# Kernel tuning notes

Hardware: AMD Instinct MI355X
Metric: run time of the kernel (lower is better)

The kernel has to match this reference:

```python
import jax, jax.numpy as jnp
import numpy as np

D = 1024      # embed_dim
E = 2048      # expand * embed_dim
S_DIM = 128   # shrunken attn dim s
C = 256       # chunk size
SRC = 4096    # src_len
G = SRC // C  # num chunks
B = 8
STD = 0.02


def setup_inputs() -> dict:
    key = jax.random.key(0)
    ks = jax.random.split(key, 16)
    n = lambda k, shp: jax.random.normal(k, shp, dtype=jnp.float32)
    inp = {
        "query": n(ks[0], (SRC, B, D)),
        "key":   n(ks[1], (SRC, B, D)),
        "value": n(ks[2], (SRC, B, D)),
        # learned params (torch Linear stored as [in, out])
        "Wxs": n(ks[3], (D, S_DIM)) * STD, "bxs": n(ks[4], (S_DIM,)) * STD,
        "Wve": n(ks[5], (D, E)) * STD,     "bve": n(ks[6], (E,)) * STD,
        "Wue": n(ks[7], (D, E)) * STD,     "bue": n(ks[8], (E,)) * STD,
        "Wod": n(ks[9], (E, D)) * STD,     "bod": n(ks[10], (D,)) * STD,
        "rel_bias": n(ks[11], (C,)) * STD,
        "gamma": n(ks[12], (4, S_DIM)) * STD,
        "beta":  n(ks[13], (4, S_DIM)) * STD,
    }
    return inp


def reference(query, key, value, Wxs, bxs, Wve, bve, Wue, bue, Wod, bod,
              rel_bias, gamma, beta):
    # [S, B, D] -> [B, G, C, D]
    x = jnp.transpose(value, (1, 0, 2)).reshape(B, G, C, D)
    v = jnp.tanh(x @ Wve + bve)          # [b,g,c,e]
    z = jnp.tanh(x @ Wxs + bxs)          # [b,g,c,s]
    q_quad = z * gamma[0] + beta[0]
    k_quad = z * gamma[1] + beta[1]
    q_lin  = z * gamma[2] + beta[2]
    k_lin  = z * gamma[3] + beta[3]
    # local quadratic attention: relu(qk + bias)^2
    qk = jnp.einsum('bgns,bgms->bgnm', q_quad, k_quad)
    a = jnp.square(jax.nn.relu(qk + rel_bias))
    v_quad = jnp.einsum('bgnm,bgme->bgne', a, v)
    # global linear attention
    kv = jnp.einsum('bgcs,bgce->bse', k_lin, v)
    v_lin = jnp.einsum('bgcs,bse->bgce', q_lin, kv)
    u = jnp.tanh(x @ Wue + bue)          # [b,g,c,e]
    o = (u * (v_quad + v_lin)) @ Wod + bod   # [b,g,c,d]
    o = o.reshape(B, G * C, D)
    return jnp.transpose(o, (1, 0, 2))   # [S, B, D]
```

## Files before the change

kernel.cpp:

```cpp
#include <hip/hip_runtime.h>
#include <hip/hip_bf16.h>

using u16 = unsigned short;
using u32 = unsigned int;

typedef __attribute__((ext_vector_type(8))) short bf8;
typedef __attribute__((ext_vector_type(4))) float f4;
typedef __attribute__((ext_vector_type(4))) u16  us4;

#define DEV static __device__ __forceinline__

DEV float bf2f(u16 u) { return __uint_as_float(((u32)u) << 16); }
DEV u16 f2bf(float f) {
    u32 x = __float_as_uint(f);
    x += 0x7FFFu + ((x >> 16) & 1u);
    return (u16)(x >> 16);
}
DEV float tanhf_fast(float x) {
    float e = __expf(2.0f * x);
    return 1.0f - 2.0f / (e + 1.0f);
}
DEV f4 MFMA(bf8 a, bf8 b, f4 c) {
    return __builtin_amdgcn_mfma_f32_16x16x32_bf16(a, b, c, 0, 0, 0);
}
DEV int xcd_swz(int bx, int nwg) { return (bx & 7) * (nwg >> 3) + (bx >> 3); }

DEV void gload16(const u16* src, u16* dst) {
    __builtin_amdgcn_global_load_lds(
        (const __attribute__((address_space(1))) void*)src,
        (__attribute__((address_space(3))) void*)dst, 16, 0, 0);
}

#define SBAR()  __builtin_amdgcn_s_barrier()
#define SCHED() __builtin_amdgcn_sched_barrier(0)


#define WS_XB    ((size_t)0)
#define WS_WXST  ((size_t)67108864)
#define WS_WVET  ((size_t)67371008)
#define WS_WUET  ((size_t)71565312)
#define WS_WODT  ((size_t)75759616)
#define WS_KVT   ((size_t)79953920)
#define WS_A     ((size_t)84148224)
#define WS_QL    ((size_t)100925440)
#define WS_VT    ((size_t)109314048)
#define WS_T1    ((size_t)243531776)
#define WS_Z     ((size_t)243531776)
#define WS_KLT   ((size_t)251920384)
#define WS_QQ    ((size_t)260308992)
#define WS_KQ    ((size_t)268697600)
#define WS_KVF   ((size_t)277086208)

DEV void stage128x64(const u16* __restrict__ gbase, int ld, u16* lds, int w, int lane) {
    const int srow = lane >> 3;
    const int scol = ((lane & 7) ^ srow) * 8;
    #pragma unroll
    for (int i = 0; i < 4; i++) {
        const int rt = (i * 4 + w) * 8 + srow;
        gload16(gbase + (size_t)rt * ld + scol, lds + (size_t)(i * 4 + w) * 512);
    }
}

DEV void frag_mfma_64_swz(const u16* As, const u16* Bs, int wm, int wn, int ln, int lh,
                          f4 acc[4][4]) {
    #pragma unroll
    for (int kk2 = 0; kk2 < 2; kk2++) {
        const int sx = (((kk2 << 2) + lh) ^ (ln & 7)) << 3;
        bf8 a[4], b[4];
        #pragma unroll
        for (int mt = 0; mt < 4; mt++)
            a[mt] = *reinterpret_cast<const bf8*>(As + (wm * 64 + mt * 16 + ln) * 64 + sx);
        #pragma unroll
        for (int nt = 0; nt < 4; nt++)
            b[nt] = *reinterpret_cast<const bf8*>(Bs + (wn * 64 + nt * 16 + ln) * 64 + sx);
        #pragma unroll
        for (int mt = 0; mt < 4; mt++)
            #pragma unroll
            for (int nt = 0; nt < 4; nt++)
                acc[mt][nt] = MFMA(a[mt], b[nt], acc[mt][nt]);
    }
}

template<int NT, typename FA, typename FB>
DEV void gemm_pipe(FA stageA, FB stageB, u16* As, u16* Bs,
                   int wm, int wn, int ln, int lh, f4 acc[4][4]) {
    stageA(As, 0); stageB(Bs, 0);
    #pragma unroll 2
    for (int t = 0; t + 1 < NT; ++t) {
        u16* An = As + ((t & 1) ^ 1) * 8192;
        u16* Bn = Bs + ((t & 1) ^ 1) * 8192;
        stageA(An, t + 1); stageB(Bn, t + 1);
        asm volatile("s_waitcnt vmcnt(8)" ::: "memory");
        SBAR(); SCHED();
        frag_mfma_64_swz(As + (t & 1) * 8192, Bs + (t & 1) * 8192, wm, wn, ln, lh, acc);
        SCHED(); SBAR(); SCHED();
    }
    asm volatile("s_waitcnt vmcnt(0)" ::: "memory");
    SBAR();
    frag_mfma_64_swz(As + ((NT - 1) & 1) * 8192, Bs + ((NT - 1) & 1) * 8192, wm, wn, ln, lh, acc);
    SBAR();
}


#define T256 16384

DEV void stage2(const u16* __restrict__ gbase, int ld, u16* lds, int tid, int i0, int i1) {
    const int slot = tid & 7;
    {
        const int row = i0 * 64 + (tid >> 3);
        gload16(gbase + (size_t)row * ld + ((slot ^ (row & 7)) << 3),
                lds + ((size_t)(i0 * 512 + (tid & ~63)) << 3));
    }
    {
        const int row = i1 * 64 + (tid >> 3);
        gload16(gbase + (size_t)row * ld + ((slot ^ (row & 7)) << 3),
                lds + ((size_t)(i1 * 512 + (tid & ~63)) << 3));
    }
}

DEV const bf8* frag_ptr(const u16* base, int row, int ks, int lh) {
    const int slot = ((ks << 2) + lh) ^ (row & 7);
    return reinterpret_cast<const bf8*>(base + row * 64 + slot * 8);
}

template<int NT, typename FA, typename FB>
DEV void gemm_pipe8(FA sA, FB sB, u16* As, u16* Bs,
                    int wm, int wn, int ln, int lh, f4 acc[8][4]) {
    sA(As, 0, 0, 2); sA(As, 0, 1, 3); sB(Bs, 0, 0, 1); sB(Bs, 0, 2, 3);
    if (NT > 1) {
        sA(As + T256, 1, 0, 2); sA(As + T256, 1, 1, 3);
        sB(Bs + T256, 1, 0, 1); sB(Bs + T256, 1, 2, 3);
        asm volatile("s_waitcnt vmcnt(8)" ::: "memory");
    } else {
        asm volatile("s_waitcnt vmcnt(0)" ::: "memory");
    }
    SBAR(); SCHED();
    #pragma unroll 2
    for (int t = 0; t < NT; ++t) {
        const int c = t & 1;
        const u16* Ab = As + c * T256;
        const u16* Bb = Bs + c * T256;
        u16* Ac = As + c * T256;
        u16* Bc = Bs + c * T256;
        bf8 aR[8], b0[4], b1[4];
        #pragma unroll
        for (int j = 0; j < 4; j++) {
            aR[j]     = *frag_ptr(Ab, wm * 128 + j * 16 + ln, 0, lh);
            aR[4 + j] = *frag_ptr(Ab, wm * 128 + j * 16 + ln, 1, lh);
        }
        #pragma unroll
        for (int k = 0; k < 2; k++) {
            b0[k]     = *frag_ptr(Bb, wn * 64 + k * 16 + ln, 0, lh);
            b0[2 + k] = *frag_ptr(Bb, wn * 64 + k * 16 + ln, 1, lh);
        }
        SBAR(); SCHED();
        __builtin_amdgcn_s_setprio(1);
        #pragma unroll
        for (int j = 0; j < 4; j++) { acc[j][0] = MFMA(aR[j], b0[0], acc[j][0]);
                                      acc[j][1] = MFMA(aR[j], b0[1], acc[j][1]); }
        #pragma unroll
        for (int j = 0; j < 4; j++) { acc[j][0] = MFMA(aR[4 + j], b0[2], acc[j][0]);
                                      acc[j][1] = MFMA(aR[4 + j], b0[3], acc[j][1]); }
        __builtin_amdgcn_s_setprio(0);
        SCHED();
        #pragma unroll
        for (int k = 0; k < 2; k++) {
            b1[k]     = *frag_ptr(Bb, wn * 64 + (2 + k) * 16 + ln, 0, lh);
            b1[2 + k] = *frag_ptr(Bb, wn * 64 + (2 + k) * 16 + ln, 1, lh);
        }
        SBAR(); SCHED();
        __builtin_amdgcn_s_setprio(1);
        #pragma unroll
        for (int j = 0; j < 4; j++) { acc[j][2] = MFMA(aR[j], b1[0], acc[j][2]);
                                      acc[j][3] = MFMA(aR[j], b1[1], acc[j][3]); }
        #pragma unroll
        for (int j = 0; j < 4; j++) { acc[j][2] = MFMA(aR[4 + j], b1[2], acc[j][2]);
                                      acc[j][3] = MFMA(aR[4 + j], b1[3], acc[j][3]); }
        __builtin_amdgcn_s_setprio(0);
        SCHED();
        #pragma unroll
        for (int j = 0; j < 4; j++) {
            aR[j]     = *frag_ptr(Ab, wm * 128 + 64 + j * 16 + ln, 0, lh);
            aR[4 + j] = *frag_ptr(Ab, wm * 128 + 64 + j * 16 + ln, 1, lh);
        }
        if (t + 2 < NT) { sA(Ac, t + 2, 0, 2); sB(Bc, t + 2, 0, 1); }
        SBAR(); SCHED();
        __builtin_amdgcn_s_setprio(1);
        #pragma unroll
        for (int j = 0; j < 4; j++) { acc[4 + j][0] = MFMA(aR[j], b0[0], acc[4 + j][0]);
                                      acc[4 + j][1] = MFMA(aR[j], b0[1], acc[4 + j][1]); }
        #pragma unroll
        for (int j = 0; j < 4; j++) { acc[4 + j][0] = MFMA(aR[4 + j], b0[2], acc[4 + j][0]);
                                      acc[4 + j][1] = MFMA(aR[4 + j], b0[3], acc[4 + j][1]); }
        __builtin_amdgcn_s_setprio(0);
        SCHED();
        if (t + 2 < NT) {
            sA(Ac, t + 2, 1, 3); sB(Bc, t + 2, 2, 3);
            asm volatile("s_waitcnt vmcnt(8)" ::: "memory");
        } else if (t + 1 < NT) {
            asm volatile("s_waitcnt vmcnt(0)" ::: "memory");
        }
        SBAR(); SCHED();
        __builtin_amdgcn_s_setprio(1);
        #pragma unroll
        for (int j = 0; j < 4; j++) { acc[4 + j][2] = MFMA(aR[j], b1[0], acc[4 + j][2]);
                                      acc[4 + j][3] = MFMA(aR[j], b1[1], acc[4 + j][3]); }
        #pragma unroll
        for (int j = 0; j < 4; j++) { acc[4 + j][2] = MFMA(aR[4 + j], b1[2], acc[4 + j][2]);
                                      acc[4 + j][3] = MFMA(aR[4 + j], b1[3], acc[4 + j][3]); }
        __builtin_amdgcn_s_setprio(0);
        SCHED();
    }
}

__global__ void k_cvt_x(const float* __restrict__ src, u16* __restrict__ dst) {
    int m = blockIdx.x;
    int s = m >> 3, b = m & 7;
    const float* in = src + (size_t)m * 1024;
    u16* outp = dst + (((size_t)b << 12) + s) * 1024;
    int t = threadIdx.x * 4;
    float4 v = *reinterpret_cast<const float4*>(in + t);
    us4 o; o[0] = f2bf(v.x); o[1] = f2bf(v.y); o[2] = f2bf(v.z); o[3] = f2bf(v.w);
    *reinterpret_cast<us4*>(outp + t) = o;
}

__global__ void k_transpose(const float* __restrict__ src, u16* __restrict__ dst, int R, int C) {
    __shared__ u16 tile[32][33];
    int tx = threadIdx.x & 31, ty = threadIdx.x >> 5;
    int r0 = blockIdx.y * 32, c0 = blockIdx.x * 32;
    #pragma unroll
    for (int rr = ty; rr < 32; rr += 8)
        tile[rr][tx] = f2bf(src[(size_t)(r0 + rr) * C + c0 + tx]);
    __syncthreads();
    #pragma unroll
    for (int cc = ty; cc < 32; cc += 8)
        dst[(size_t)(c0 + cc) * R + r0 + tx] = tile[tx][cc];
}

__global__ void k_klinT(const u16* __restrict__ z, const float* __restrict__ gamma,
                        const float* __restrict__ beta, u16* __restrict__ klt) {
    __shared__ u16 tile[32][33];
    int tx = threadIdx.x & 31, ty = threadIdx.x >> 5;
    int r0 = blockIdx.x * 32;
    int c0 = blockIdx.y * 32;
    float gs = gamma[384 + c0 + tx], bs = beta[384 + c0 + tx];
    #pragma unroll
    for (int rr = ty; rr < 32; rr += 8) {
        u16 zv = z[(size_t)(r0 + rr) * 128 + c0 + tx];
        tile[rr][tx] = f2bf(bf2f(zv) * gs + bs);
    }
    __syncthreads();
    int b = r0 >> 12;
    int pos0 = r0 & 4095;
    #pragma unroll
    for (int cc = ty; cc < 32; cc += 8)
        klt[(((size_t)b * 128 + c0 + cc) << 12) + pos0 + tx] = tile[tx][cc];
}

__global__ __launch_bounds__(256) void k_zgemm(const u16* __restrict__ xb, const u16* __restrict__ WxsT,
                                               const float* __restrict__ bxs,
                                               const float* __restrict__ gamma, const float* __restrict__ beta,
                                               u16* __restrict__ z, u16* __restrict__ qq,
                                               u16* __restrict__ kq, u16* __restrict__ ql) {
    __shared__ u16 As[2][128 * 64];
    __shared__ u16 Bs[2][128 * 64];
    const int tid = threadIdx.x;
    const int lane = tid & 63, w = tid >> 6;
    const int ln = lane & 15, lh = lane >> 4;
    const int wm = w >> 1, wn = w & 1;
    const int rowbase = xcd_swz(blockIdx.x, 256) * 128;
    const u16* Ab = xb + (size_t)rowbase * 1024;
    f4 acc[4][4] = {};
    gemm_pipe<16>(
        [&](u16* l, int t) { stage128x64(Ab + t * 64, 1024, l, w, lane); },
        [&](u16* l, int t) { stage128x64(WxsT + t * 64, 1024, l, w, lane); },
        As[0], Bs[0], wm, wn, ln, lh, acc);
    #pragma unroll
    for (int mt = 0; mt < 4; mt++)
        #pragma unroll
        for (int nt = 0; nt < 4; nt++) {
            int col = wn * 64 + nt * 16 + ln;
            float bias = bxs[col];
            float g0 = gamma[col],       b0 = beta[col];
            float g1 = gamma[128 + col], b1 = beta[128 + col];
            float g2 = gamma[256 + col], b2 = beta[256 + col];
            int r0 = rowbase + wm * 64 + mt * 16 + lh * 4;
            #pragma unroll
            for (int rg = 0; rg < 4; rg++) {
                float zv = tanhf_fast(acc[mt][nt][rg] + bias);
                size_t idx = ((size_t)(r0 + rg) << 7) + col;
                z[idx]  = f2bf(zv);
                qq[idx] = f2bf(zv * g0 + b0);
                kq[idx] = f2bf(zv * g1 + b1);
                ql[idx] = f2bf(zv * g2 + b2);
            }
        }
}

__global__ __launch_bounds__(512, 2) void k_vgemm(const u16* __restrict__ xb, const u16* __restrict__ WveT,
                                                  const float* __restrict__ bve, u16* __restrict__ vT) {
    __shared__ u16 As[2 * T256];
    __shared__ u16 Bs[2 * T256];
    const int tid = threadIdx.x;
    const int lane = tid & 63, w = tid >> 6;
    const int ln = lane & 15, lh = lane >> 4;
    const int wm = w >> 2, wn = w & 3;
    const int rowbase = blockIdx.y * 256;
    const int colbase = blockIdx.x * 256;
    const u16* Ag = xb + (size_t)rowbase * 1024;
    const u16* Bg = WveT + (size_t)colbase * 1024;
    f4 acc[8][4] = {};
    gemm_pipe8<16>(
        [&](u16* l, int t, int i0, int i1) { stage2(Ag + t * 64, 1024, l, tid, i0, i1); },
        [&](u16* l, int t, int i0, int i1) { stage2(Bg + t * 64, 1024, l, tid, i0, i1); },
        As, Bs, wm, wn, ln, lh, acc);
    #pragma unroll
    for (int mt = 0; mt < 8; mt++)
        #pragma unroll
        for (int nt = 0; nt < 4; nt++) {
            int e = colbase + wn * 64 + nt * 16 + ln;
            float bias = bve[e];
            int r0 = rowbase + wm * 128 + mt * 16 + lh * 4;
            int bb = r0 >> 12, s0 = r0 & 4095;
            us4 p;
            #pragma unroll
            for (int rg = 0; rg < 4; rg++) p[rg] = f2bf(tanhf_fast(acc[mt][nt][rg] + bias));
            *reinterpret_cast<us4*>(vT + (((size_t)bb * 2048 + e) << 12) + s0) = p;
        }
}

__global__ __launch_bounds__(256) void k_kv(const u16* __restrict__ vT, const u16* __restrict__ klt,
                                            float* __restrict__ kvF) {
    __shared__ u16 As[2][128 * 64];
    __shared__ u16 Bs[2][128 * 64];
    const int tid = threadIdx.x;
    const int lane = tid & 63, w = tid >> 6;
    const int ln = lane & 15, lh = lane >> 4;
    const int wm = w >> 1, wn = w & 1;
    const int b = blockIdx.z;
    const int rowbase = blockIdx.x * 128;
    const int kbase = blockIdx.y * 1024;
    const u16* Ab = vT + ((size_t)b * 2048 + rowbase) * 4096 + kbase;
    const u16* Bb = klt + ((size_t)b * 128) * 4096 + kbase;
    f4 acc[4][4] = {};
    gemm_pipe<16>(
        [&](u16* l, int t) { stage128x64(Ab + t * 64, 4096, l, w, lane); },
        [&](u16* l, int t) { stage128x64(Bb + t * 64, 4096, l, w, lane); },
        As[0], Bs[0], wm, wn, ln, lh, acc);
    #pragma unroll
    for (int mt = 0; mt < 4; mt++)
        #pragma unroll
        for (int nt = 0; nt < 4; nt++) {
            int s = wn * 64 + nt * 16 + ln;
            int e0 = rowbase + wm * 64 + mt * 16 + lh * 4;
            #pragma unroll
            for (int rg = 0; rg < 4; rg++)
                atomicAdd(&kvF[(((size_t)b * 2048 + e0 + rg) << 7) + s], acc[mt][nt][rg]);
        }
}

__global__ void k_kvcvt(const float* __restrict__ kvF, u16* __restrict__ kvT, int n) {
    int i = (blockIdx.x * blockDim.x + threadIdx.x) * 4;
    if (i < n) {
        float4 v = *reinterpret_cast<const float4*>(kvF + i);
        us4 o; o[0] = f2bf(v.x); o[1] = f2bf(v.y); o[2] = f2bf(v.z); o[3] = f2bf(v.w);
        *reinterpret_cast<us4*>(kvT + i) = o;
    }
}

__global__ __launch_bounds__(256) void k_a(const u16* __restrict__ qq, const u16* __restrict__ kq,
                                           const float* __restrict__ rel_bias, u16* __restrict__ a_out) {
    const int lane = threadIdx.x & 63, wid = threadIdx.x >> 6;
    const int ln = lane & 15, lh = lane >> 4;
    const int wm = wid >> 1, wn = wid & 1;
    const int ci = blockIdx.y;
    const int qbase = blockIdx.x * 128 + wm * 64;
    const int nbase = wn * 128;
    const int rowbase = ci << 8;
    f4 acc[4][8] = {};
    const u16* qr[4];
    #pragma unroll
    for (int mt = 0; mt < 4; mt++) qr[mt] = qq + ((size_t)(rowbase + qbase + mt * 16 + ln) << 7);
    const u16* kr[8];
    #pragma unroll
    for (int nt = 0; nt < 8; nt++) kr[nt] = kq + ((size_t)(rowbase + nbase + nt * 16 + ln) << 7);
    #pragma unroll
    for (int kk = 0; kk < 128; kk += 32) {
        int k0 = kk + lh * 8;
        bf8 aq[4], ak[8];
        #pragma unroll
        for (int mt = 0; mt < 4; mt++) aq[mt] = *reinterpret_cast<const bf8*>(qr[mt] + k0);
        #pragma unroll
        for (int nt = 0; nt < 8; nt++) ak[nt] = *reinterpret_cast<const bf8*>(kr[nt] + k0);
        #pragma unroll
        for (int mt = 0; mt < 4; mt++)
            #pragma unroll
            for (int nt = 0; nt < 8; nt++)
                acc[mt][nt] = MFMA(aq[mt], ak[nt], acc[mt][nt]);
    }
    #pragma unroll
    for (int nt = 0; nt < 8; nt++) {
        int key = nbase + nt * 16 + ln;
        float rb = rel_bias[key];
        #pragma unroll
        for (int mt = 0; mt < 4; mt++) {
            int r0 = qbase + mt * 16 + lh * 4;
            #pragma unroll
            for (int rg = 0; rg < 4; rg++) {
                float v = acc[mt][nt][rg] + rb;
                v = fmaxf(v, 0.0f); v = v * v;
                a_out[((size_t)ci << 16) + ((size_t)(r0 + rg) << 8) + key] = f2bf(v);
            }
        }
    }
}

__global__ __launch_bounds__(512, 2) void k_t1(const u16* __restrict__ ql, const u16* __restrict__ a_in,
                                               const u16* __restrict__ vT, const u16* __restrict__ kvT,
                                               u16* __restrict__ t1) {
    __shared__ u16 As[2 * T256];
    __shared__ u16 Bs[2 * T256];
    const int tid = threadIdx.x;
    const int lane = tid & 63, w = tid >> 6;
    const int ln = lane & 15, lh = lane >> 4;
    const int wm = w >> 2, wn = w & 3;
    const int ci = xcd_swz(blockIdx.x, 128);
    const int rowbase = ci << 8;
    const int ebase = blockIdx.y * 256;
    const int b = ci >> 4, g = ci & 15;
    const u16* Aa = ql + (size_t)rowbase * 128;
    const u16* Ba = kvT + ((size_t)(b * 2048 + ebase)) * 128;
    const u16* Ab2 = a_in + ((size_t)ci << 16);
    const u16* Bb2 = vT + ((size_t)(b * 2048 + ebase)) * 4096 + (g << 8);
    f4 acc[8][4] = {};
    gemm_pipe8<6>(
        [&](u16* l, int t, int i0, int i1) {
            if (t < 2) stage2(Aa + t * 64, 128, l, tid, i0, i1);
            else       stage2(Ab2 + (t - 2) * 64, 256, l, tid, i0, i1);
        },
        [&](u16* l, int t, int i0, int i1) {
            if (t < 2) stage2(Ba + t * 64, 128, l, tid, i0, i1);
            else       stage2(Bb2 + (t - 2) * 64, 4096, l, tid, i0, i1);
        },
        As, Bs, wm, wn, ln, lh, acc);
    #pragma unroll
    for (int mt = 0; mt < 8; mt++)
        #pragma unroll
        for (int nt = 0; nt < 4; nt++) {
            int e = ebase + wn * 64 + nt * 16 + ln;
            int r0 = rowbase + wm * 128 + mt * 16 + lh * 4;
            #pragma unroll
            for (int rg = 0; rg < 4; rg++)
                t1[((size_t)(r0 + rg) << 11) + e] = f2bf(acc[mt][nt][rg]);
        }
}

__global__ __launch_bounds__(512, 2) void k_u(const u16* __restrict__ xb, const u16* __restrict__ WueT,
                                              const float* __restrict__ bue, u16* t1) {
    __shared__ u16 As[2 * T256];
    __shared__ u16 Bs[2 * T256];
    const int tid = threadIdx.x;
    const int lane = tid & 63, w = tid >> 6;
    const int ln = lane & 15, lh = lane >> 4;
    const int wm = w >> 2, wn = w & 3;
    const int rowbase = blockIdx.y * 256;
    const int colbase = blockIdx.x * 256;
    const u16* Ag = xb + (size_t)rowbase * 1024;
    const u16* Bg = WueT + (size_t)colbase * 1024;
    f4 acc[8][4] = {};
    gemm_pipe8<16>(
        [&](u16* l, int t, int i0, int i1) { stage2(Ag + t * 64, 1024, l, tid, i0, i1); },
        [&](u16* l, int t, int i0, int i1) { stage2(Bg + t * 64, 1024, l, tid, i0, i1); },
        As, Bs, wm, wn, ln, lh, acc);
    #pragma unroll
    for (int mt = 0; mt < 8; mt++)
        #pragma unroll
        for (int nt = 0; nt < 4; nt++) {
            int e = colbase + wn * 64 + nt * 16 + ln;
            float bias = bue[e];
            int r0 = rowbase + wm * 128 + mt * 16 + lh * 4;
            #pragma unroll
            for (int rg = 0; rg < 4; rg++) {
                size_t idx = ((size_t)(r0 + rg) << 11) + e;
                float t = bf2f(t1[idx]);
                float u = tanhf_fast(acc[mt][nt][rg] + bias);
                t1[idx] = f2bf(u * t);
            }
        }
}

__global__ __launch_bounds__(512, 2) void k_o(const u16* __restrict__ t1, const u16* __restrict__ WodT,
                                              const float* __restrict__ bod, float* __restrict__ out) {
    __shared__ u16 As[2 * T256];
    __shared__ u16 Bs[2 * T256];
    const int tid = threadIdx.x;
    const int lane = tid & 63, w = tid >> 6;
    const int ln = lane & 15, lh = lane >> 4;
    const int wm = w >> 2, wn = w & 3;
    const int rowbase = blockIdx.y * 256;
    const int colbase = blockIdx.x * 256;
    const u16* Ag = t1 + (size_t)rowbase * 2048;
    const u16* Bg = WodT + (size_t)colbase * 2048;
    f4 acc[8][4] = {};
    gemm_pipe8<32>(
        [&](u16* l, int t, int i0, int i1) { stage2(Ag + t * 64, 2048, l, tid, i0, i1); },
        [&](u16* l, int t, int i0, int i1) { stage2(Bg + t * 64, 2048, l, tid, i0, i1); },
        As, Bs, wm, wn, ln, lh, acc);
    #pragma unroll
    for (int mt = 0; mt < 8; mt++)
        #pragma unroll
        for (int nt = 0; nt < 4; nt++) {
            int d = colbase + wn * 64 + nt * 16 + ln;
            float bias = bod[d];
            int r0 = rowbase + wm * 128 + mt * 16 + lh * 4;
            #pragma unroll
            for (int rg = 0; rg < 4; rg++) {
                int r = r0 + rg;
                int s = r & 4095, bb = r >> 12;
                out[((size_t)(s * 8 + bb) << 10) + d] = acc[mt][nt][rg] + bias;
            }
        }
}

extern "C" void kernel_launch(void* const* d_in, const int* in_sizes, int n_in,
                              void* d_out, int out_size, void* d_ws, size_t ws_size,
                              hipStream_t stream) {
    const float* value = (const float*)d_in[2];
    const float* Wxs = (const float*)d_in[3];  const float* bxs = (const float*)d_in[4];
    const float* Wve = (const float*)d_in[5];  const float* bve = (const float*)d_in[6];
    const float* Wue = (const float*)d_in[7];  const float* bue = (const float*)d_in[8];
    const float* Wod = (const float*)d_in[9];  const float* bod = (const float*)d_in[10];
    const float* rel_bias = (const float*)d_in[11];
    const float* gamma = (const float*)d_in[12];
    const float* beta  = (const float*)d_in[13];
    float* out = (float*)d_out;

    char* ws = (char*)d_ws;
    u16* xb   = (u16*)(ws + WS_XB);
    u16* WxsT = (u16*)(ws + WS_WXST);
    u16* WveT = (u16*)(ws + WS_WVET);
    u16* WueT = (u16*)(ws + WS_WUET);
    u16* WodT = (u16*)(ws + WS_WODT);
    u16* kvT  = (u16*)(ws + WS_KVT);
    u16* a    = (u16*)(ws + WS_A);
    u16* ql   = (u16*)(ws + WS_QL);
    u16* vT   = (u16*)(ws + WS_VT);
    u16* t1   = (u16*)(ws + WS_T1);
    u16* z    = (u16*)(ws + WS_Z);
    u16* klt  = (u16*)(ws + WS_KLT);
    u16* qq   = (u16*)(ws + WS_QQ);
    u16* kq   = (u16*)(ws + WS_KQ);
    float* kvF = (float*)(ws + WS_KVF);

    k_cvt_x<<<32768, 256, 0, stream>>>(value, xb);
    k_transpose<<<dim3(4, 32),  256, 0, stream>>>(Wxs, WxsT, 1024, 128);
    k_transpose<<<dim3(64, 32), 256, 0, stream>>>(Wve, WveT, 1024, 2048);
    k_transpose<<<dim3(64, 32), 256, 0, stream>>>(Wue, WueT, 1024, 2048);
    k_transpose<<<dim3(32, 64), 256, 0, stream>>>(Wod, WodT, 2048, 1024);
    k_zgemm<<<256, 256, 0, stream>>>(xb, WxsT, bxs, gamma, beta, z, qq, kq, ql);
    k_klinT<<<dim3(1024, 4), 256, 0, stream>>>(z, gamma, beta, klt);
    k_vgemm<<<dim3(8, 128), 512, 0, stream>>>(xb, WveT, bve, vT);
    hipMemsetAsync(kvF, 0, (size_t)8 * 2048 * 128 * 4, stream);
    k_kv<<<dim3(16, 4, 8), 256, 0, stream>>>(vT, klt, kvF);
    k_kvcvt<<<2048, 256, 0, stream>>>(kvF, kvT, 8 * 2048 * 128);
    k_a<<<dim3(2, 128), 256, 0, stream>>>(qq, kq, rel_bias, a);
    k_t1<<<dim3(128, 8), 512, 0, stream>>>(ql, a, vT, kvT, t1);
    k_u<<<dim3(8, 128), 512, 0, stream>>>(xb, WueT, bue, t1);
    k_o<<<dim3(4, 128), 512, 0, stream>>>(t1, WodT, bod, out);
}
```

Measured before the change: 731.0 us.

## Fuse attention-output and U-gate GEMMs into one kernel with 128-row tiles

Merges the k_t1 kernel (v_quad + v_lin GEMM) and the k_u kernel (tanh(x·Wue+b) gating) into a single k_t1u kernel. The block keeps both accumulators in registers and writes the gated product once, so t1 is no longer written, read back and rewritten in global memory. To fit both accumulators, the M tile drops from 256 to 128 rows, using a new gemm_pipe8f pipeline with a smaller A buffer, and the grid doubles to 2048 blocks. The cost is more register pressure, lower arithmetic intensity per block, and redundant loads of the B tiles (kvT, vT, WueT) across row blocks.

```diff
diff --git a/kernel.cpp b/kernel.cpp
--- a/kernel.cpp
+++ b/kernel.cpp
@@ -101,21 +101,18 @@
     SBAR();
 }
 
-
 #define T256 16384
 
+DEV void stageQ(const u16* __restrict__ gbase, int ld, u16* lds, int tid, int q) {
+    const int slot = tid & 7;
+    const int row = q * 64 + (tid >> 3);
+    gload16(gbase + (size_t)row * ld + ((slot ^ (row & 7)) << 3),
+            lds + ((size_t)(q * 512 + (tid & ~63)) << 3));
+}
+
 DEV void stage2(const u16* __restrict__ gbase, int ld, u16* lds, int tid, int i0, int i1) {
-    const int slot = tid & 7;
-    {
-        const int row = i0 * 64 + (tid >> 3);
-        gload16(gbase + (size_t)row * ld + ((slot ^ (row & 7)) << 3),
-                lds + ((size_t)(i0 * 512 + (tid & ~63)) << 3));
-    }
-    {
-        const int row = i1 * 64 + (tid >> 3);
-        gload16(gbase + (size_t)row * ld + ((slot ^ (row & 7)) << 3),
-                lds + ((size_t)(i1 * 512 + (tid & ~63)) << 3));
-    }
+    stageQ(gbase, ld, lds, tid, i0);
+    stageQ(gbase, ld, lds, tid, i1);
 }
 
 DEV const bf8* frag_ptr(const u16* base, int row, int ks, int lh) {
@@ -208,6 +205,94 @@
         #pragma unroll
         for (int j = 0; j < 4; j++) { acc[4 + j][2] = MFMA(aR[4 + j], b1[2], acc[4 + j][2]);
                                       acc[4 + j][3] = MFMA(aR[4 + j], b1[3], acc[4 + j][3]); }
+        __builtin_amdgcn_s_setprio(0);
+        SCHED();
+    }
+}
+
+#define TA128 8192
+
+template<int NT, typename FA, typename FB>
+DEV void gemm_pipe8f(FA sA, FB sB, u16* As, u16* Bs,
+                     int wm, int wn, int ln, int lh, f4 acc[4][4]) {
+    sA(As, 0, 0); sA(As, 0, 1); sB(Bs, 0, 0, 1); sB(Bs, 0, 2, 3);
+    if (NT > 1) {
+        sA(As + TA128, 1, 0); sA(As + TA128, 1, 1);
+        sB(Bs + T256, 1, 0, 1); sB(Bs + T256, 1, 2, 3);
+        asm volatile("s_waitcnt vmcnt(6)" ::: "memory");
+    } else {
+        asm volatile("s_waitcnt vmcnt(0)" ::: "memory");
+    }
+    SBAR(); SCHED();
+    #pragma unroll 2
+    for (int t = 0; t < NT; ++t) {
+        const int c = t & 1;
+        const u16* Ab = As + c * TA128;
+        const u16* Bb = Bs + c * T256;
+        u16* Ac = As + c * TA128;
+        u16* Bc = Bs + c * T256;
+        bf8 aR[8], b0[4], b1[4];
+        #pragma unroll
+        for (int j = 0; j < 2; j++) {
+            aR[j]     = *frag_ptr(Ab, wm * 64 + j * 16 + ln, 0, lh);
+            aR[2 + j] = *frag_ptr(Ab, wm * 64 + j * 16 + ln, 1, lh);
+        }
+        #pragma unroll
+        for (int k = 0; k < 2; k++) {
+            b0[k]     = *frag_ptr(Bb, wn * 64 + k * 16 + ln, 0, lh);
+            b0[2 + k] = *frag_ptr(Bb, wn * 64 + k * 16 + ln, 1, lh);
+        }
+        SBAR(); SCHED();
+        __builtin_amdgcn_s_setprio(1);
+        #pragma unroll
+        for (int j = 0; j < 2; j++) { acc[j][0] = MFMA(aR[j], b0[0], acc[j][0]);
+                                      acc[j][1] = MFMA(aR[j], b0[1], acc[j][1]);
+                                      acc[j][0] = MFMA(aR[2 + j], b0[2], acc[j][0]);
+                                      acc[j][1] = MFMA(aR[2 + j], b0[3], acc[j][1]); }
+        __builtin_amdgcn_s_setprio(0);
+        SCHED();
+        #pragma unroll
+        for (int k = 0; k < 2; k++) {
+            b1[k]     = *frag_ptr(Bb, wn * 64 + (2 + k) * 16 + ln, 0, lh);
+            b1[2 + k] = *frag_ptr(Bb, wn * 64 + (2 + k) * 16 + ln, 1, lh);
+        }
+        SBAR(); SCHED();
+        __builtin_amdgcn_s_setprio(1);
+        #pragma unroll
+        for (int j = 0; j < 2; j++) { acc[j][2] = MFMA(aR[j], b1[0], acc[j][2]);
+                                      acc[j][3] = MFMA(aR[j], b1[1], acc[j][3]);
+                                      acc[j][2] = MFMA(aR[2 + j], b1[2], acc[j][2]);
+                                      acc[j][3] = MFMA(aR[2 + j], b1[3], acc[j][3]); }
+        __builtin_amdgcn_s_setprio(0);
+        SCHED();
+        #pragma unroll
+        for (int j = 0; j < 2; j++) {
+            aR[4 + j] = *frag_ptr(Ab, wm * 64 + (2 + j) * 16 + ln, 0, lh);
+            aR[6 + j] = *frag_ptr(Ab, wm * 64 + (2 + j) * 16 + ln, 1, lh);
+        }
+        if (t + 2 < NT) sB(Bc, t + 2, 0, 1);
+        SBAR(); SCHED();
+        __builtin_amdgcn_s_setprio(1);
+        #pragma unroll
+        for (int j = 0; j < 2; j++) { acc[2 + j][0] = MFMA(aR[4 + j], b0[0], acc[2 + j][0]);
+                                      acc[2 + j][1] = MFMA(aR[4 + j], b0[1], acc[2 + j][1]);
+                                      acc[2 + j][0] = MFMA(aR[6 + j], b0[2], acc[2 + j][0]);
+                                      acc[2 + j][1] = MFMA(aR[6 + j], b0[3], acc[2 + j][1]); }
+        __builtin_amdgcn_s_setprio(0);
+        SCHED();
+        if (t + 2 < NT) {
+            sA(Ac, t + 2, 0); sA(Ac, t + 2, 1); sB(Bc, t + 2, 2, 3);
+            asm volatile("s_waitcnt vmcnt(6)" ::: "memory");
+        } else if (t + 1 < NT) {
+            asm volatile("s_waitcnt vmcnt(0)" ::: "memory");
+        }
+        SBAR(); SCHED();
+        __builtin_amdgcn_s_setprio(1);
+        #pragma unroll
+        for (int j = 0; j < 2; j++) { acc[2 + j][2] = MFMA(aR[4 + j], b1[0], acc[2 + j][2]);
+                                      acc[2 + j][3] = MFMA(aR[4 + j], b1[1], acc[2 + j][3]);
+                                      acc[2 + j][2] = MFMA(aR[6 + j], b1[2], acc[2 + j][2]);
+                                      acc[2 + j][3] = MFMA(aR[6 + j], b1[3], acc[2 + j][3]); }
         __builtin_amdgcn_s_setprio(0);
         SCHED();
     }
@@ -415,76 +500,59 @@
     }
 }
 
-__global__ __launch_bounds__(512, 2) void k_t1(const u16* __restrict__ ql, const u16* __restrict__ a_in,
-                                               const u16* __restrict__ vT, const u16* __restrict__ kvT,
-                                               u16* __restrict__ t1) {
-    __shared__ u16 As[2 * T256];
+__global__ __launch_bounds__(512, 2) void k_t1u(const u16* __restrict__ ql, const u16* __restrict__ a_in,
+                                                const u16* __restrict__ vT, const u16* __restrict__ kvT,
+                                                const u16* __restrict__ xb, const u16* __restrict__ WueT,
+                                                const float* __restrict__ bue, u16* __restrict__ t1) {
+    __shared__ u16 As[2 * TA128];
     __shared__ u16 Bs[2 * T256];
     const int tid = threadIdx.x;
     const int lane = tid & 63, w = tid >> 6;
     const int ln = lane & 15, lh = lane >> 4;
     const int wm = w >> 2, wn = w & 3;
-    const int ci = xcd_swz(blockIdx.x, 128);
-    const int rowbase = ci << 8;
-    const int ebase = blockIdx.y * 256;
-    const int b = ci >> 4, g = ci & 15;
-    const u16* Aa = ql + (size_t)rowbase * 128;
-    const u16* Ba = kvT + ((size_t)(b * 2048 + ebase)) * 128;
-    const u16* Ab2 = a_in + ((size_t)ci << 16);
+    const int rowbase = blockIdx.y * 128;
+    const int ebase = blockIdx.x * 256;
+    const int ci = rowbase >> 8, g = ci & 15, b = ci >> 4;
+    const int lqbase = rowbase & 255;
+
+    const u16* Aa  = ql + (size_t)rowbase * 128;
+    const u16* Ba  = kvT + ((size_t)(b * 2048 + ebase)) * 128;
+    const u16* Ab2 = a_in + ((size_t)ci << 16) + (size_t)lqbase * 256;
     const u16* Bb2 = vT + ((size_t)(b * 2048 + ebase)) * 4096 + (g << 8);
-    f4 acc[8][4] = {};
-    gemm_pipe8<6>(
-        [&](u16* l, int t, int i0, int i1) {
-            if (t < 2) stage2(Aa + t * 64, 128, l, tid, i0, i1);
-            else       stage2(Ab2 + (t - 2) * 64, 256, l, tid, i0, i1);
+
+    f4 acc[4][4] = {};
+    gemm_pipe8f<6>(
+        [&](u16* l, int t, int q) {
+            if (t < 2) stageQ(Aa + t * 64, 128, l, tid, q);
+            else       stageQ(Ab2 + (t - 2) * 64, 256, l, tid, q);
         },
         [&](u16* l, int t, int i0, int i1) {
             if (t < 2) stage2(Ba + t * 64, 128, l, tid, i0, i1);
             else       stage2(Bb2 + (t - 2) * 64, 4096, l, tid, i0, i1);
         },
         As, Bs, wm, wn, ln, lh, acc);
-    #pragma unroll
-    for (int mt = 0; mt < 8; mt++)
+
+    SBAR();
+
+    const u16* Ag = xb + (size_t)rowbase * 1024;
+    const u16* Bg = WueT + (size_t)ebase * 1024;
+    f4 accu[4][4] = {};
+    gemm_pipe8f<16>(
+        [&](u16* l, int t, int q) { stageQ(Ag + t * 64, 1024, l, tid, q); },
+        [&](u16* l, int t, int i0, int i1) { stage2(Bg + t * 64, 1024, l, tid, i0, i1); },
+        As, Bs, wm, wn, ln, lh, accu);
+
+    #pragma unroll
+    for (int mt = 0; mt < 4; mt++)
         #pragma unroll
         for (int nt = 0; nt < 4; nt++) {
             int e = ebase + wn * 64 + nt * 16 + ln;
-            int r0 = rowbase + wm * 128 + mt * 16 + lh * 4;
-            #pragma unroll
-            for (int rg = 0; rg < 4; rg++)
-                t1[((size_t)(r0 + rg) << 11) + e] = f2bf(acc[mt][nt][rg]);
-        }
-}
-
-__global__ __launch_bounds__(512, 2) void k_u(const u16* __restrict__ xb, const u16* __restrict__ WueT,
-                                              const float* __restrict__ bue, u16* t1) {
-    __shared__ u16 As[2 * T256];
-    __shared__ u16 Bs[2 * T256];
-    const int tid = threadIdx.x;
-    const int lane = tid & 63, w = tid >> 6;
-    const int ln = lane & 15, lh = lane >> 4;
-    const int wm = w >> 2, wn = w & 3;
-    const int rowbase = blockIdx.y * 256;
-    const int colbase = blockIdx.x * 256;
-    const u16* Ag = xb + (size_t)rowbase * 1024;
-    const u16* Bg = WueT + (size_t)colbase * 1024;
-    f4 acc[8][4] = {};
-    gemm_pipe8<16>(
-        [&](u16* l, int t, int i0, int i1) { stage2(Ag + t * 64, 1024, l, tid, i0, i1); },
-        [&](u16* l, int t, int i0, int i1) { stage2(Bg + t * 64, 1024, l, tid, i0, i1); },
-        As, Bs, wm, wn, ln, lh, acc);
-    #pragma unroll
-    for (int mt = 0; mt < 8; mt++)
-        #pragma unroll
-        for (int nt = 0; nt < 4; nt++) {
-            int e = colbase + wn * 64 + nt * 16 + ln;
             float bias = bue[e];
-            int r0 = rowbase + wm * 128 + mt * 16 + lh * 4;
+            int r0 = rowbase + wm * 64 + mt * 16 + lh * 4;
             #pragma unroll
             for (int rg = 0; rg < 4; rg++) {
-                size_t idx = ((size_t)(r0 + rg) << 11) + e;
-                float t = bf2f(t1[idx]);
-                float u = tanhf_fast(acc[mt][nt][rg] + bias);
-                t1[idx] = f2bf(u * t);
+                float uu = tanhf_fast(accu[mt][nt][rg] + bias);
+                t1[((size_t)(r0 + rg) << 11) + e] = f2bf(uu * acc[mt][nt][rg]);
             }
         }
 }
@@ -564,7 +632,6 @@
     k_kv<<<dim3(16, 4, 8), 256, 0, stream>>>(vT, klt, kvF);
     k_kvcvt<<<2048, 256, 0, stream>>>(kvF, kvT, 8 * 2048 * 128);
     k_a<<<dim3(2, 128), 256, 0, stream>>>(qq, kq, rel_bias, a);
-    k_t1<<<dim3(128, 8), 512, 0, stream>>>(ql, a, vT, kvT, t1);
-    k_u<<<dim3(8, 128), 512, 0, stream>>>(xb, WueT, bue, t1);
+    k_t1u<<<dim3(8, 256), 512, 0, stream>>>(ql, a, vT, kvT, xb, WueT, bue, t1);
     k_o<<<dim3(4, 128), 512, 0, stream>>>(t1, WodT, bod, out);
 }
```

Result: no change. 739.1 us (+1.1%).
